# Kernel tuning notes

Measured on AMD Instinct MI355X. Metric: run time of the kernel, lower is better.

Reference implementation:

```python
import jax, jax.numpy as jnp
import numpy as np
from jax import lax

# 8-neighbor zero-pad offsets as (left, right, top, bottom), matching nn.ZeroPad2d args
PADS = [(0, 2, 0, 2), (1, 1, 0, 2), (2, 0, 0, 2), (0, 2, 1, 1),
        (2, 0, 1, 1), (0, 2, 2, 0), (1, 1, 2, 0), (2, 0, 2, 0)]
BN_EPS = 1e-5


def conv2d(x, w, pad):
    return lax.conv_general_dilated(x, w, (1, 1), [(pad, pad), (pad, pad)],
                                    dimension_numbers=('NCHW', 'OIHW', 'NCHW'))


def batchnorm(x, gamma, beta, mean, var):
    inv = gamma * lax.rsqrt(var + BN_EPS)
    return x * inv[None, :, None, None] + (beta - mean * inv)[None, :, None, None]


def resize_bilinear(x, oh, ow):
    # F.interpolate(mode='bilinear', align_corners=False)
    n, c, h, w = x.shape
    ys = jnp.clip((jnp.arange(oh, dtype=x.dtype) + 0.5) * (h / oh) - 0.5, 0.0, None)
    xs = jnp.clip((jnp.arange(ow, dtype=x.dtype) + 0.5) * (w / ow) - 0.5, 0.0, None)
    y0 = jnp.floor(ys); x0 = jnp.floor(xs)
    wy = (ys - y0)[:, None]; wx = (xs - x0)[None, :]
    y0i = jnp.clip(y0.astype(jnp.int32), 0, h - 1)
    y1i = jnp.clip(y0i + 1, 0, h - 1)
    x0i = jnp.clip(x0.astype(jnp.int32), 0, w - 1)
    x1i = jnp.clip(x0i + 1, 0, w - 1)
    r0 = x[:, :, y0i, :]; r1 = x[:, :, y1i, :]
    top = r0[:, :, :, x0i] * (1 - wx) + r0[:, :, :, x1i] * wx
    bot = r1[:, :, :, x0i] * (1 - wx) + r1[:, :, :, x1i] * wx
    return top * (1 - wy) + bot * wy


def lrwarp_error(left, disp, right):
    # Warp right image toward left using horizontal disparity (bilinear,
    # zero padding outside), then per-channel absolute photometric error.
    n, c, h, w = right.shape
    xs = jnp.arange(w, dtype=disp.dtype)[None, None, None, :] - disp  # [n,1,h,w]
    x0 = jnp.floor(xs)
    frac = xs - x0
    x0i = x0.astype(jnp.int32)
    x1i = x0i + 1
    v0 = ((x0i >= 0) & (x0i < w)).astype(right.dtype)
    v1 = ((x1i >= 0) & (x1i < w)).astype(right.dtype)
    x0c = jnp.broadcast_to(jnp.clip(x0i, 0, w - 1), (n, c, h, w))
    x1c = jnp.broadcast_to(jnp.clip(x1i, 0, w - 1), (n, c, h, w))
    g0 = jnp.take_along_axis(right, x0c, axis=3) * v0
    g1 = jnp.take_along_axis(right, x1c, axis=3) * v1
    warped = g0 * (1 - frac) + g1 * frac
    return jnp.abs(left - warped)


def setup_inputs() -> dict:
    key = jax.random.key(0)
    ks = jax.random.split(key, 16)
    N, H, W = 8, 256, 256
    inp = {
        'normal_estimation': jax.random.normal(ks[0], (N, 3, H, W), jnp.float32),
        'left_image': jax.random.uniform(ks[1], (N, 3, 512, 512), jnp.float32),
        'right_image': jax.random.uniform(ks[2], (N, 3, 512, 512), jnp.float32),
        'coarse_disparity': jax.random.uniform(ks[3], (N, 1, H, W), jnp.float32),
        'w1': jax.random.normal(ks[4], (32, 12, 3, 3), jnp.float32) * 0.1,
        'g1': jnp.ones((32,), jnp.float32), 'b1': jnp.zeros((32,), jnp.float32),
        'm1': jax.random.normal(ks[5], (32,), jnp.float32) * 0.01,
        'v1': jax.random.uniform(ks[6], (32,), jnp.float32, 0.5, 1.5),
        'w2': jax.random.normal(ks[7], (64, 32, 3, 3), jnp.float32) * 0.1,
        'g2': jnp.ones((64,), jnp.float32), 'b2': jnp.zeros((64,), jnp.float32),
        'm2': jax.random.normal(ks[8], (64,), jnp.float32) * 0.01,
        'v2': jax.random.uniform(ks[9], (64,), jnp.float32, 0.5, 1.5),
        'w3': jax.random.normal(ks[10], (8, 64, 1, 1), jnp.float32) * 0.1,
    }
    return inp


def _forward(normal_estimation, left_image, right_image, coarse_disparity,
             w1, g1, b1, m1, v1, w2, g2, b2, m2, v2, w3):
    H, W = coarse_disparity.shape[-2], coarse_disparity.shape[-1]
    cur_l = resize_bilinear(left_image, H, W)
    cur_r = resize_bilinear(right_image, H, W)
    disp_err = lrwarp_error(cur_l, coarse_disparity, cur_r)
    feats = jnp.concatenate([normal_estimation, cur_l, cur_r, disp_err], axis=1)
    x = jax.nn.relu(batchnorm(conv2d(feats, w1, 1), g1, b1, m1, v1))
    x = jax.nn.relu(batchnorm(conv2d(x, w2, 1), g2, b2, m2, v2))
    aff = jax.nn.relu(conv2d(x, w3, 0))  # [N,8,H,W]
    gate_p = jnp.stack([jnp.pad(aff[:, k], ((0, 0), (t, b), (l, r)))
                        for k, (l, r, t, b) in enumerate(PADS)], axis=1)
    d = coarse_disparity[:, 0]
    disp_p = jnp.stack([jnp.pad(d, ((0, 0), (t, b), (l, r)))
                        for (l, r, t, b) in PADS], axis=1)
    gate = jax.nn.softmax(gate_p, axis=1)
    prop = jnp.sum(gate * disp_p, axis=1, keepdims=True)[:, :, 1:-1, 1:-1]
    return prop * 0.3 + coarse_disparity * 0.7


def reference(normal_estimation, left_image, right_image, coarse_disparity,
              w1, g1, b1, m1, v1, w2, g2, b2, m2, v2, w3):
    return _forward(normal_estimation, left_image, right_image, coarse_disparity,
                    w1, g1, b1, m1, v1, w2, g2, b2, m2, v2, w3)
```

## Files before the change

### kernel.cpp

```cpp
#include <hip/hip_runtime.h>
#include <math.h>

#define NB 8
#define HH 256
#define WW 256
#define HW (HH*WW)

#define OFF_FEATS 0UL
#define OFF_X1B   16777216UL
#define OFF_AFFB  50331648UL
#define OFF_W1FB  58720256UL
#define OFF_B1FB  58732544UL
#define OFF_W2FB  58732672UL
#define OFF_B2FB  58769536UL
#define OFF_W3FB  58769792UL

typedef short  short8 __attribute__((ext_vector_type(8)));
typedef ushort u16x8  __attribute__((ext_vector_type(8)));
typedef ushort u16x4  __attribute__((ext_vector_type(4)));
typedef float  f32x4  __attribute__((ext_vector_type(4)));

__device__ __forceinline__ ushort f2bf(float x) {
  uint u = __float_as_uint(x);
  return (ushort)((u + 0x7FFFu + ((u >> 16) & 1u)) >> 16);
}
__device__ __forceinline__ float bf2f(ushort h) {
  uint u = ((uint)h) << 16;
  return __uint_as_float(u);
}

__global__ __launch_bounds__(256) void build_feats(
    const float* __restrict__ normal, const float* __restrict__ left,
    const float* __restrict__ right, const float* __restrict__ disp,
    const float* __restrict__ w1, const float* __restrict__ g1,
    const float* __restrict__ b1, const float* __restrict__ m1,
    const float* __restrict__ v1,
    const float* __restrict__ w2, const float* __restrict__ g2,
    const float* __restrict__ b2, const float* __restrict__ m2,
    const float* __restrict__ v2, const float* __restrict__ w3,
    char* __restrict__ wsb) {
  if (blockIdx.x >= 1024) {
    int idx = (blockIdx.x - 1024) * 256 + threadIdx.x;
    ushort* w1f = (ushort*)(wsb + OFF_W1FB);
    float* b1f  = (float*)(wsb + OFF_B1FB);
    ushort* w2f = (ushort*)(wsb + OFF_W2FB);
    float* b2f  = (float*)(wsb + OFF_B2FB);
    ushort* w3f = (ushort*)(wsb + OFF_W3FB);
    if (idx < 6144) {
      int jj = idx & 7;
      int lane = (idx >> 3) & 63;
      int mt = (idx >> 9) & 1;
      int s = idx >> 10;
      int ky = s >> 1, t = s & 1;
      int q = lane >> 4, lx = lane & 15;
      int k = q * 8 + jj;
      int dcol = k >> 4, ch = k & 15;
      int kx = t * 2 + dcol;
      int out = mt * 16 + lx;
      float inv = g1[out] / sqrtf(v1[out] + 1e-5f);
      float val = (ch < 12 && kx < 3) ? w1[((out * 12 + ch) * 3 + ky) * 3 + kx] * inv : 0.f;
      w1f[idx] = f2bf(val);
    }
    int j = idx - 6144;
    if (j >= 0 && j < 18432) {
      int kk   = j >> 11;
      int nt   = (j >> 9) & 3;
      int lane = (j >> 3) & 63;
      int jj   = j & 7;
      int q  = lane >> 4, lx = lane & 15;
      int cin = q * 8 + jj;
      int out = nt * 16 + lx;
      float inv = g2[out] / sqrtf(v2[out] + 1e-5f);
      w2f[j] = f2bf(w2[(out * 32 + cin) * 9 + kk] * inv);
      if (kk == 0 && q == 0 && jj == 0) b2f[out] = b2[out] - m2[out] * inv;
    }
    int k2 = idx - 24576;
    if (k2 >= 0 && k2 < 32) {
      float inv = g1[k2] / sqrtf(v1[k2] + 1e-5f);
      b1f[k2] = b1[k2] - m1[k2] * inv;
    }
    int k3 = idx - 24608;
    if (k3 >= 0 && k3 < 1024) {
      int jj = k3 & 7;
      int lane = (k3 >> 3) & 63;
      int slice = k3 >> 9;
      int q = lane >> 4, lx = lane & 15;
      int ch = slice * 32 + q * 8 + jj;
      w3f[k3] = (lx < 8) ? f2bf(w3[lx * 64 + ch]) : (ushort)0;
    }
    return;
  }
  int gid = blockIdx.x * 256 + threadIdx.x;
  int n = gid >> 15;
  int r = gid & 32767;
  int i = r >> 7;
  int jt = r & 127;
  int j0 = jt << 1;
  int i2 = i << 1;
  ushort* feats = (ushort*)(wsb + OFF_FEATS);
  ushort tmp[32];
#pragma unroll
  for (int c = 0; c < 3; ++c) {
    float2 nm = *(const float2*)(normal + (size_t)(n * 3 + c) * HW + i * 256 + j0);
    tmp[c] = f2bf(nm.x);
    tmp[16 + c] = f2bf(nm.y);
  }
  float cl[2][3];
#pragma unroll
  for (int c = 0; c < 3; ++c) {
    const float* Lp = left + ((size_t)(n * 3 + c) * 512 + i2) * 512 + (j0 << 1);
    float4 a0 = *(const float4*)Lp;
    float4 a1 = *(const float4*)(Lp + 512);
    cl[0][c] = 0.25f * (a0.x + a0.y + a1.x + a1.y);
    cl[1][c] = 0.25f * (a0.z + a0.w + a1.z + a1.w);
    tmp[3 + c] = f2bf(cl[0][c]);
    tmp[19 + c] = f2bf(cl[1][c]);
    const float* Rp = right + ((size_t)(n * 3 + c) * 512 + i2) * 512 + (j0 << 1);
    float4 b0 = *(const float4*)Rp;
    float4 b1v = *(const float4*)(Rp + 512);
    tmp[6 + c] = f2bf(0.25f * (b0.x + b0.y + b1v.x + b1v.y));
    tmp[22 + c] = f2bf(0.25f * (b0.z + b0.w + b1v.z + b1v.w));
  }
  float2 dp2 = *(const float2*)(disp + (size_t)n * HW + i * 256 + j0);
#pragma unroll
  for (int p = 0; p < 2; ++p) {
    int j = j0 + p;
    float d = p ? dp2.y : dp2.x;
    float xs = (float)j - d;
    float x0f = floorf(xs);
    float fr = xs - x0f;
    int ix0 = (int)x0f;
    int ix1 = ix0 + 1;
    float vm0 = (ix0 >= 0 && ix0 < WW) ? 1.f : 0.f;
    float vm1 = (ix1 >= 0 && ix1 < WW) ? 1.f : 0.f;
    int x0c = min(max(ix0, 0), WW - 1);
    int x1c = min(max(ix1, 0), WW - 1);
    bool adj = (x1c == x0c + 1);
    int xs2 = min(x0c + 1, WW - 1);
#pragma unroll
    for (int c = 0; c < 3; ++c) {
      const float* Rb = right + ((size_t)(n * 3 + c) * 512 + i2) * 512;
      float2 f0 = *(const float2*)(Rb + (x0c << 1));
      float2 f1 = *(const float2*)(Rb + (x0c << 1) + 512);
      float2 f2v = *(const float2*)(Rb + (xs2 << 1));
      float2 f3 = *(const float2*)(Rb + (xs2 << 1) + 512);
      float avg0 = 0.25f * (f0.x + f0.y + f1.x + f1.y);
      float avg1 = 0.25f * (f2v.x + f2v.y + f3.x + f3.y);
      float gg0 = avg0 * vm0;
      float gg1 = (adj ? avg1 : avg0) * vm1;
      float warped = gg0 * (1.f - fr) + gg1 * fr;
      tmp[p * 16 + 9 + c] = f2bf(fabsf(cl[p][c] - warped));
    }
  }
#pragma unroll
  for (int c = 12; c < 16; ++c) { tmp[c] = 0; tmp[16 + c] = 0; }
  size_t ob = ((size_t)(n * HW + i * 256 + j0)) * 16;
#pragma unroll
  for (int vv = 0; vv < 4; ++vv)
    *(u16x8*)&feats[ob + vv * 8] = *(u16x8*)&tmp[vv * 8];
}

__global__ __launch_bounds__(256) void conv1_kernel(char* __restrict__ wsb) {
  __shared__ ushort tile[688 * 8];
  const ushort* __restrict__ feats = (const ushort*)(wsb + OFF_FEATS);
  const short8* __restrict__ w1fv = (const short8*)(wsb + OFF_W1FB);
  const float* __restrict__ b1f = (const float*)(wsb + OFF_B1FB);
  ushort* x1 = (ushort*)(wsb + OFF_X1B);
  int blk = blockIdx.x;
  int n = blk >> 8;
  int t = blk & 255;
  int ty0 = (t >> 4) << 4;
  int tx0 = (t & 15) << 4;
  int tid = threadIdx.x;
  int lane = tid & 63;
  int wid = tid >> 6;
  int q = lane >> 4;
  int lx = lane & 15;
  short8 aw[2][6];
#pragma unroll
  for (int s = 0; s < 6; ++s)
#pragma unroll
    for (int mt = 0; mt < 2; ++mt) aw[mt][s] = w1fv[(s * 2 + mt) * 64 + lane];
  for (int e = tid; e < 684; e += 256) {
    int row = e / 38;
    int rem = e - row * 38;
    int col = rem >> 1;
    int cc = rem & 1;
    int gy = ty0 + row - 1, gx = tx0 + col - 1;
    u16x8 v = (u16x8)0;
    if (gy >= 0 && gy < HH && gx >= 0 && gx < WW)
      v = *(const u16x8*)&feats[(((size_t)(n * 256 + gy)) * 256 + gx) * 16 + cc * 8];
    int slot = e ^ ((e >> 3) & 7);
    *(u16x8*)&tile[slot * 8] = v;
  }
  __syncthreads();
  short8 bfrag[6][2];
#pragma unroll
  for (int dr = 0; dr < 6; ++dr)
#pragma unroll
    for (int tt = 0; tt < 2; ++tt) {
      int prow = wid * 4 + dr;
      int G = (prow * 19 + lx + tt * 2 + (q >> 1)) * 2 + (q & 1);
      int slot = G ^ ((G >> 3) & 7);
      bfrag[dr][tt] = *(const short8*)&tile[slot * 8];
    }
  f32x4 acc[4][2];
#pragma unroll
  for (int rowt = 0; rowt < 4; ++rowt)
#pragma unroll
    for (int mt = 0; mt < 2; ++mt) acc[rowt][mt] = (f32x4)0.f;
#pragma unroll
  for (int s = 0; s < 6; ++s) {
    int ky = s >> 1;
    int tt = s & 1;
#pragma unroll
    for (int rowt = 0; rowt < 4; ++rowt) {
      short8 b = bfrag[rowt + ky][tt];
      acc[rowt][0] = __builtin_amdgcn_mfma_f32_16x16x32_bf16(aw[0][s], b, acc[rowt][0], 0, 0, 0);
      acc[rowt][1] = __builtin_amdgcn_mfma_f32_16x16x32_bf16(aw[1][s], b, acc[rowt][1], 0, 0, 0);
    }
  }
#pragma unroll
  for (int rowt = 0; rowt < 4; ++rowt) {
    int gy = ty0 + wid * 4 + rowt;
    int gx = tx0 + lx;
    size_t pb = (((size_t)(n * 256 + gy)) * 256 + gx) * 32;
#pragma unroll
    for (int mt = 0; mt < 2; ++mt) {
      u16x4 pack;
#pragma unroll
      for (int r = 0; r < 4; ++r) {
        int ch = mt * 16 + q * 4 + r;
        pack[r] = f2bf(fmaxf(acc[rowt][mt][r] + b1f[ch], 0.f));
      }
      *(u16x4*)&x1[pb + mt * 16 + q * 4] = pack;
    }
  }
}

__global__ __launch_bounds__(256) void conv2_kernel(char* __restrict__ wsb) {
  __shared__ ushort smem[256 * 68];
  const ushort* __restrict__ x1 = (const ushort*)(wsb + OFF_X1B);
  const short8* __restrict__ w2fv = (const short8*)(wsb + OFF_W2FB);
  const float* __restrict__ b2f = (const float*)(wsb + OFF_B2FB);
  const short8* __restrict__ w3fv = (const short8*)(wsb + OFF_W3FB);
  ushort* aff = (ushort*)(wsb + OFF_AFFB);

  int blk = blockIdx.x;
  int n = blk >> 8;
  int t = blk & 255;
  int ty0 = (t >> 4) << 4;
  int tx0 = (t & 15) << 4;
  int tid = threadIdx.x;
  int lane = tid & 63;
  int wid = tid >> 6;
  int q = lane >> 4;
  int lx = lane & 15;

  short8 bw3[2];
  bw3[0] = w3fv[lane];
  bw3[1] = w3fv[64 + lane];

  for (int e = tid; e < 1296; e += 256) {
    int p = e >> 2;
    int c = e & 3;
    int y = p / 18;
    int x = p - y * 18;
    int gy = ty0 + y - 1, gx = tx0 + x - 1;
    u16x8 val = (u16x8)0;
    if (gy >= 0 && gy < HH && gx >= 0 && gx < WW)
      val = *(const u16x8*)&x1[(((size_t)(n * 256 + gy)) * 256 + gx) * 32 + c * 8];
    *(u16x8*)&smem[p * 36 + c * 8] = val;
  }
  __syncthreads();

  f32x4 acc[4][4];
#pragma unroll
  for (int mt = 0; mt < 4; ++mt)
#pragma unroll
    for (int nt = 0; nt < 4; ++nt) acc[mt][nt] = (f32x4)0.f;

#pragma unroll
  for (int kk = 0; kk < 9; ++kk) {
    int ky = kk / 3, kx = kk - ky * 3;
    short8 a[4], b[4];
#pragma unroll
    for (int mt = 0; mt < 4; ++mt) {
      int row = wid * 4 + mt;
      a[mt] = *(const short8*)&smem[((row + ky) * 18 + lx + kx) * 36 + q * 8];
    }
#pragma unroll
    for (int nt = 0; nt < 4; ++nt) b[nt] = w2fv[(kk * 4 + nt) * 64 + lane];
#pragma unroll
    for (int mt = 0; mt < 4; ++mt)
#pragma unroll
      for (int nt = 0; nt < 4; ++nt)
        acc[mt][nt] = __builtin_amdgcn_mfma_f32_16x16x32_bf16(a[mt], b[nt], acc[mt][nt], 0, 0, 0);
  }

  __syncthreads();
#pragma unroll
  for (int nt = 0; nt < 4; ++nt) {
    float bias = b2f[nt * 16 + lx];
#pragma unroll
    for (int mt = 0; mt < 4; ++mt) {
      int row = wid * 4 + mt;
#pragma unroll
      for (int r = 0; r < 4; ++r) {
        int p = row * 16 + q * 4 + r;
        float v = fmaxf(acc[mt][nt][r] + bias, 0.f);
        smem[p * 68 + nt * 16 + lx] = f2bf(v);
      }
    }
  }
  __syncthreads();

  f32x4 acc3[4];
#pragma unroll
  for (int mt = 0; mt < 4; ++mt) acc3[mt] = (f32x4)0.f;
#pragma unroll
  for (int mt = 0; mt < 4; ++mt) {
    int p = wid * 64 + mt * 16 + lx;
#pragma unroll
    for (int s = 0; s < 2; ++s) {
      short8 a3 = *(const short8*)&smem[p * 68 + s * 32 + q * 8];
      acc3[mt] = __builtin_amdgcn_mfma_f32_16x16x32_bf16(a3, bw3[s], acc3[mt], 0, 0, 0);
    }
  }
  if (lx < 8) {
#pragma unroll
    for (int mt = 0; mt < 4; ++mt) {
      int py = ty0 + wid * 4 + mt;
      int px = tx0 + q * 4;
      u16x4 pk;
#pragma unroll
      for (int r = 0; r < 4; ++r) pk[r] = f2bf(fmaxf(acc3[mt][r], 0.f));
      *(u16x4*)&aff[((size_t)(n * 8 + lx)) * HW + (size_t)py * WW + px] = pk;
    }
  }
}

__global__ __launch_bounds__(256) void final_kernel(const float* __restrict__ disp,
                                                    const char* __restrict__ wsb,
                                                    float* __restrict__ out) {
  int gid = blockIdx.x * 256 + threadIdx.x;
  int n = gid >> 14;
  int r = gid & 16383;
  int i = r >> 6;
  int j0 = (r & 63) << 2;
  const ushort* aff = (const ushort*)(wsb + OFF_AFFB);
  float d6[3][6];
#pragma unroll
  for (int rr = 0; rr < 3; ++rr) {
    int y = min(max(i + rr - 1, 0), HH - 1);
    const float* dp = disp + (size_t)n * HW + y * WW;
    float4 c4 = *(const float4*)(dp + j0);
    d6[rr][1] = c4.x; d6[rr][2] = c4.y; d6[rr][3] = c4.z; d6[rr][4] = c4.w;
    d6[rr][0] = dp[max(j0 - 1, 0)];
    d6[rr][5] = dp[min(j0 + 4, WW - 1)];
  }
  const int dy[8] = {1, 1, 1, 0, 0, -1, -1, -1};
  const int dx[8] = {1, 0, -1, 1, -1, 1, 0, -1};
  float g[8][4], dvv[8][4];
#pragma unroll
  for (int k = 0; k < 8; ++k) {
    int y = i + dy[k];
    bool vy = (y >= 0 && y < HH);
    int yc = min(max(y, 0), HH - 1);
    const ushort* ap = aff + ((size_t)(n * 8 + k)) * HW + (size_t)yc * WW;
    float w6[6];
    u16x4 c4 = *(const u16x4*)(ap + j0);
    w6[1] = bf2f(c4[0]); w6[2] = bf2f(c4[1]); w6[3] = bf2f(c4[2]); w6[4] = bf2f(c4[3]);
    w6[0] = bf2f(ap[max(j0 - 1, 0)]);
    w6[5] = bf2f(ap[min(j0 + 4, WW - 1)]);
    int rr = dy[k] + 1;
#pragma unroll
    for (int p = 0; p < 4; ++p) {
      int xp = j0 + p + dx[k];
      bool ok = vy && (xp >= 0) && (xp < WW);
      g[k][p] = ok ? w6[p + 1 + dx[k]] : 0.f;
      dvv[k][p] = ok ? d6[rr][p + 1 + dx[k]] : 0.f;
    }
  }
  float4 res;
#pragma unroll
  for (int p = 0; p < 4; ++p) {
    float m = g[0][p];
#pragma unroll
    for (int k = 1; k < 8; ++k) m = fmaxf(m, g[k][p]);
    float se = 0.f, sed = 0.f;
#pragma unroll
    for (int k = 0; k < 8; ++k) {
      float e = __expf(g[k][p] - m);
      se += e;
      sed += e * dvv[k][p];
    }
    float dc = d6[1][p + 1];
    (&res.x)[p] = 0.3f * (sed / se) + 0.7f * dc;
  }
  *(float4*)(out + (size_t)n * HW + i * WW + j0) = res;
}

extern "C" void kernel_launch(void* const* d_in, const int* in_sizes, int n_in,
                              void* d_out, int out_size, void* d_ws, size_t ws_size,
                              hipStream_t stream) {
  const float* normal = (const float*)d_in[0];
  const float* left   = (const float*)d_in[1];
  const float* right  = (const float*)d_in[2];
  const float* disp   = (const float*)d_in[3];
  const float* w1 = (const float*)d_in[4];
  const float* g1 = (const float*)d_in[5];
  const float* b1 = (const float*)d_in[6];
  const float* m1 = (const float*)d_in[7];
  const float* v1 = (const float*)d_in[8];
  const float* w2 = (const float*)d_in[9];
  const float* g2 = (const float*)d_in[10];
  const float* b2 = (const float*)d_in[11];
  const float* m2 = (const float*)d_in[12];
  const float* v2 = (const float*)d_in[13];
  const float* w3 = (const float*)d_in[14];
  char* wsb  = (char*)d_ws;
  float* out = (float*)d_out;

  hipLaunchKernelGGL(build_feats, dim3(1125), dim3(256), 0, stream,
                     normal, left, right, disp,
                     w1, g1, b1, m1, v1, w2, g2, b2, m2, v2, w3, wsb);
  hipLaunchKernelGGL(conv1_kernel, dim3(2048), dim3(256), 0, stream, wsb);
  hipLaunchKernelGGL(conv2_kernel, dim3(2048), dim3(256), 0, stream, wsb);
  hipLaunchKernelGGL(final_kernel, dim3(512), dim3(256), 0, stream, disp, wsb, out);
}
```

Before: 166.5 us.

## Fuse feature build, conv1 and conv2 into one tiled trunk kernel

Merges feature construction, conv1 and conv2/conv3 into a single per-tile kernel. Each block computes its features over a 20x20 halo region, runs conv1 over an 18x18 region into LDS, then applies conv2 and conv3 from shared memory. Weight preparation moves to its own small kernel. This removes the global round trips for the 16-channel feats and 32-channel x1 intermediates, plus one launch. The cost is recomputing halo features and conv1 outputs at tile borders, more LDS per block, and uncoalesced scalar gathers of the input images.

New measurement: 169.0 us. About the same (+1.5%).

```diff
diff --git a/kernel.cpp b/kernel.cpp
--- a/kernel.cpp
+++ b/kernel.cpp
@@ -6,14 +6,12 @@
 #define WW 256
 #define HW (HH*WW)
 
-#define OFF_FEATS 0UL
-#define OFF_X1B   16777216UL
-#define OFF_AFFB  50331648UL
-#define OFF_W1FB  58720256UL
-#define OFF_B1FB  58732544UL
-#define OFF_W2FB  58732672UL
-#define OFF_B2FB  58769536UL
-#define OFF_W3FB  58769792UL
+#define OFF_AFFB  0UL
+#define OFF_W1FB  8388608UL
+#define OFF_B1FB  8400896UL
+#define OFF_W2FB  8401024UL
+#define OFF_B2FB  8437888UL
+#define OFF_W3FB  8438144UL
 
 typedef short  short8 __attribute__((ext_vector_type(8)));
 typedef ushort u16x8  __attribute__((ext_vector_type(8)));
@@ -29,9 +27,7 @@
   return __uint_as_float(u);
 }
 
-__global__ __launch_bounds__(256) void build_feats(
-    const float* __restrict__ normal, const float* __restrict__ left,
-    const float* __restrict__ right, const float* __restrict__ disp,
+__global__ __launch_bounds__(256) void prep_weights(
     const float* __restrict__ w1, const float* __restrict__ g1,
     const float* __restrict__ b1, const float* __restrict__ m1,
     const float* __restrict__ v1,
@@ -39,133 +35,69 @@
     const float* __restrict__ b2, const float* __restrict__ m2,
     const float* __restrict__ v2, const float* __restrict__ w3,
     char* __restrict__ wsb) {
-  if (blockIdx.x >= 1024) {
-    int idx = (blockIdx.x - 1024) * 256 + threadIdx.x;
-    ushort* w1f = (ushort*)(wsb + OFF_W1FB);
-    float* b1f  = (float*)(wsb + OFF_B1FB);
-    ushort* w2f = (ushort*)(wsb + OFF_W2FB);
-    float* b2f  = (float*)(wsb + OFF_B2FB);
-    ushort* w3f = (ushort*)(wsb + OFF_W3FB);
-    if (idx < 6144) {
-      int jj = idx & 7;
-      int lane = (idx >> 3) & 63;
-      int mt = (idx >> 9) & 1;
-      int s = idx >> 10;
-      int ky = s >> 1, t = s & 1;
-      int q = lane >> 4, lx = lane & 15;
-      int k = q * 8 + jj;
-      int dcol = k >> 4, ch = k & 15;
-      int kx = t * 2 + dcol;
-      int out = mt * 16 + lx;
-      float inv = g1[out] / sqrtf(v1[out] + 1e-5f);
-      float val = (ch < 12 && kx < 3) ? w1[((out * 12 + ch) * 3 + ky) * 3 + kx] * inv : 0.f;
-      w1f[idx] = f2bf(val);
-    }
-    int j = idx - 6144;
-    if (j >= 0 && j < 18432) {
-      int kk   = j >> 11;
-      int nt   = (j >> 9) & 3;
-      int lane = (j >> 3) & 63;
-      int jj   = j & 7;
-      int q  = lane >> 4, lx = lane & 15;
-      int cin = q * 8 + jj;
-      int out = nt * 16 + lx;
-      float inv = g2[out] / sqrtf(v2[out] + 1e-5f);
-      w2f[j] = f2bf(w2[(out * 32 + cin) * 9 + kk] * inv);
-      if (kk == 0 && q == 0 && jj == 0) b2f[out] = b2[out] - m2[out] * inv;
-    }
-    int k2 = idx - 24576;
-    if (k2 >= 0 && k2 < 32) {
-      float inv = g1[k2] / sqrtf(v1[k2] + 1e-5f);
-      b1f[k2] = b1[k2] - m1[k2] * inv;
-    }
-    int k3 = idx - 24608;
-    if (k3 >= 0 && k3 < 1024) {
-      int jj = k3 & 7;
-      int lane = (k3 >> 3) & 63;
-      int slice = k3 >> 9;
-      int q = lane >> 4, lx = lane & 15;
-      int ch = slice * 32 + q * 8 + jj;
-      w3f[k3] = (lx < 8) ? f2bf(w3[lx * 64 + ch]) : (ushort)0;
-    }
-    return;
-  }
-  int gid = blockIdx.x * 256 + threadIdx.x;
-  int n = gid >> 15;
-  int r = gid & 32767;
-  int i = r >> 7;
-  int jt = r & 127;
-  int j0 = jt << 1;
-  int i2 = i << 1;
-  ushort* feats = (ushort*)(wsb + OFF_FEATS);
-  ushort tmp[32];
-#pragma unroll
-  for (int c = 0; c < 3; ++c) {
-    float2 nm = *(const float2*)(normal + (size_t)(n * 3 + c) * HW + i * 256 + j0);
-    tmp[c] = f2bf(nm.x);
-    tmp[16 + c] = f2bf(nm.y);
-  }
-  float cl[2][3];
-#pragma unroll
-  for (int c = 0; c < 3; ++c) {
-    const float* Lp = left + ((size_t)(n * 3 + c) * 512 + i2) * 512 + (j0 << 1);
-    float4 a0 = *(const float4*)Lp;
-    float4 a1 = *(const float4*)(Lp + 512);
-    cl[0][c] = 0.25f * (a0.x + a0.y + a1.x + a1.y);
-    cl[1][c] = 0.25f * (a0.z + a0.w + a1.z + a1.w);
-    tmp[3 + c] = f2bf(cl[0][c]);
-    tmp[19 + c] = f2bf(cl[1][c]);
-    const float* Rp = right + ((size_t)(n * 3 + c) * 512 + i2) * 512 + (j0 << 1);
-    float4 b0 = *(const float4*)Rp;
-    float4 b1v = *(const float4*)(Rp + 512);
-    tmp[6 + c] = f2bf(0.25f * (b0.x + b0.y + b1v.x + b1v.y));
-    tmp[22 + c] = f2bf(0.25f * (b0.z + b0.w + b1v.z + b1v.w));
-  }
-  float2 dp2 = *(const float2*)(disp + (size_t)n * HW + i * 256 + j0);
-#pragma unroll
-  for (int p = 0; p < 2; ++p) {
-    int j = j0 + p;
-    float d = p ? dp2.y : dp2.x;
-    float xs = (float)j - d;
-    float x0f = floorf(xs);
-    float fr = xs - x0f;
-    int ix0 = (int)x0f;
-    int ix1 = ix0 + 1;
-    float vm0 = (ix0 >= 0 && ix0 < WW) ? 1.f : 0.f;
-    float vm1 = (ix1 >= 0 && ix1 < WW) ? 1.f : 0.f;
-    int x0c = min(max(ix0, 0), WW - 1);
-    int x1c = min(max(ix1, 0), WW - 1);
-    bool adj = (x1c == x0c + 1);
-    int xs2 = min(x0c + 1, WW - 1);
-#pragma unroll
-    for (int c = 0; c < 3; ++c) {
-      const float* Rb = right + ((size_t)(n * 3 + c) * 512 + i2) * 512;
-      float2 f0 = *(const float2*)(Rb + (x0c << 1));
-      float2 f1 = *(const float2*)(Rb + (x0c << 1) + 512);
-      float2 f2v = *(const float2*)(Rb + (xs2 << 1));
-      float2 f3 = *(const float2*)(Rb + (xs2 << 1) + 512);
-      float avg0 = 0.25f * (f0.x + f0.y + f1.x + f1.y);
-      float avg1 = 0.25f * (f2v.x + f2v.y + f3.x + f3.y);
-      float gg0 = avg0 * vm0;
-      float gg1 = (adj ? avg1 : avg0) * vm1;
-      float warped = gg0 * (1.f - fr) + gg1 * fr;
-      tmp[p * 16 + 9 + c] = f2bf(fabsf(cl[p][c] - warped));
-    }
-  }
-#pragma unroll
-  for (int c = 12; c < 16; ++c) { tmp[c] = 0; tmp[16 + c] = 0; }
-  size_t ob = ((size_t)(n * HW + i * 256 + j0)) * 16;
-#pragma unroll
-  for (int vv = 0; vv < 4; ++vv)
-    *(u16x8*)&feats[ob + vv * 8] = *(u16x8*)&tmp[vv * 8];
-}
-
-__global__ __launch_bounds__(256) void conv1_kernel(char* __restrict__ wsb) {
-  __shared__ ushort tile[688 * 8];
-  const ushort* __restrict__ feats = (const ushort*)(wsb + OFF_FEATS);
+  int idx = blockIdx.x * 256 + threadIdx.x;
+  ushort* w1f = (ushort*)(wsb + OFF_W1FB);
+  float* b1f  = (float*)(wsb + OFF_B1FB);
+  ushort* w2f = (ushort*)(wsb + OFF_W2FB);
+  float* b2f  = (float*)(wsb + OFF_B2FB);
+  ushort* w3f = (ushort*)(wsb + OFF_W3FB);
+  if (idx < 6144) {
+    int jj = idx & 7;
+    int lane = (idx >> 3) & 63;
+    int nt = (idx >> 9) & 1;
+    int s = idx >> 10;
+    int ky = s >> 1, t = s & 1;
+    int q = lane >> 4, lx = lane & 15;
+    int k = q * 8 + jj;
+    int dcol = k >> 4, ch = k & 15;
+    int kx = t * 2 + dcol;
+    int out = nt * 16 + lx;
+    float inv = g1[out] / sqrtf(v1[out] + 1e-5f);
+    float val = (ch < 12 && kx < 3) ? w1[((out * 12 + ch) * 3 + ky) * 3 + kx] * inv : 0.f;
+    w1f[idx] = f2bf(val);
+  }
+  int j = idx - 6144;
+  if (j >= 0 && j < 18432) {
+    int kk   = j >> 11;
+    int nt   = (j >> 9) & 3;
+    int lane = (j >> 3) & 63;
+    int jj   = j & 7;
+    int q  = lane >> 4, lx = lane & 15;
+    int cin = q * 8 + jj;
+    int out = nt * 16 + lx;
+    float inv = g2[out] / sqrtf(v2[out] + 1e-5f);
+    w2f[j] = f2bf(w2[(out * 32 + cin) * 9 + kk] * inv);
+    if (kk == 0 && q == 0 && jj == 0) b2f[out] = b2[out] - m2[out] * inv;
+  }
+  int k2 = idx - 24576;
+  if (k2 >= 0 && k2 < 32) {
+    float inv = g1[k2] / sqrtf(v1[k2] + 1e-5f);
+    b1f[k2] = b1[k2] - m1[k2] * inv;
+  }
+  int k3 = idx - 24608;
+  if (k3 >= 0 && k3 < 1024) {
+    int jj = k3 & 7;
+    int lane = (k3 >> 3) & 63;
+    int slice = k3 >> 9;
+    int q = lane >> 4, lx = lane & 15;
+    int ch = slice * 32 + q * 8 + jj;
+    w3f[k3] = (lx < 8) ? f2bf(w3[lx * 64 + ch]) : (ushort)0;
+  }
+}
+
+__global__ __launch_bounds__(256) void trunk_kernel(
+    const float* __restrict__ normal, const float* __restrict__ left,
+    const float* __restrict__ right, const float* __restrict__ disp,
+    char* __restrict__ wsb) {
+  __shared__ ushort buf[18304];
+  ushort* x1t = buf + 6464;
   const short8* __restrict__ w1fv = (const short8*)(wsb + OFF_W1FB);
   const float* __restrict__ b1f = (const float*)(wsb + OFF_B1FB);
-  ushort* x1 = (ushort*)(wsb + OFF_X1B);
+  const short8* __restrict__ w2fv = (const short8*)(wsb + OFF_W2FB);
+  const float* __restrict__ b2f = (const float*)(wsb + OFF_B2FB);
+  const short8* __restrict__ w3fv = (const short8*)(wsb + OFF_W3FB);
+  ushort* aff = (ushort*)(wsb + OFF_AFFB);
+
   int blk = blockIdx.x;
   int n = blk >> 8;
   int t = blk & 255;
@@ -176,145 +108,152 @@
   int wid = tid >> 6;
   int q = lane >> 4;
   int lx = lane & 15;
-  short8 aw[2][6];
-#pragma unroll
-  for (int s = 0; s < 6; ++s)
-#pragma unroll
-    for (int mt = 0; mt < 2; ++mt) aw[mt][s] = w1fv[(s * 2 + mt) * 64 + lane];
-  for (int e = tid; e < 684; e += 256) {
-    int row = e / 38;
-    int rem = e - row * 38;
-    int col = rem >> 1;
-    int cc = rem & 1;
-    int gy = ty0 + row - 1, gx = tx0 + col - 1;
-    u16x8 v = (u16x8)0;
-    if (gy >= 0 && gy < HH && gx >= 0 && gx < WW)
-      v = *(const u16x8*)&feats[(((size_t)(n * 256 + gy)) * 256 + gx) * 16 + cc * 8];
-    int slot = e ^ ((e >> 3) & 7);
-    *(u16x8*)&tile[slot * 8] = v;
+
+  if (tid < 8) *(u16x8*)&buf[(800 + tid) * 8] = (u16x8)0;
+  for (int e = tid; e < 400; e += 256) {
+    int row = e / 20, col = e - row * 20;
+    int gy = ty0 + row - 2, gx = tx0 + col - 2;
+    ushort tmp[16];
+#pragma unroll
+    for (int c = 12; c < 16; ++c) tmp[c] = 0;
+    if (gy >= 0 && gy < HH && gx >= 0 && gx < WW) {
+#pragma unroll
+      for (int c = 0; c < 3; ++c)
+        tmp[c] = f2bf(normal[(size_t)(n * 3 + c) * HW + gy * WW + gx]);
+      int i2 = gy << 1, j2 = gx << 1;
+      float cl[3];
+#pragma unroll
+      for (int c = 0; c < 3; ++c) {
+        const float* Lp = left + ((size_t)(n * 3 + c) * 512 + i2) * 512 + j2;
+        float2 a0 = *(const float2*)Lp;
+        float2 a1 = *(const float2*)(Lp + 512);
+        cl[c] = 0.25f * (a0.x + a0.y + a1.x + a1.y);
+        tmp[3 + c] = f2bf(cl[c]);
+        const float* Rp = right + ((size_t)(n * 3 + c) * 512 + i2) * 512 + j2;
+        float2 b0 = *(const float2*)Rp;
+        float2 b1v = *(const float2*)(Rp + 512);
+        tmp[6 + c] = f2bf(0.25f * (b0.x + b0.y + b1v.x + b1v.y));
+      }
+      float d = disp[(size_t)n * HW + gy * WW + gx];
+      float xs = (float)gx - d;
+      float x0f = floorf(xs);
+      float fr = xs - x0f;
+      int ix0 = (int)x0f;
+      int ix1 = ix0 + 1;
+      float vm0 = (ix0 >= 0 && ix0 < WW) ? 1.f : 0.f;
+      float vm1 = (ix1 >= 0 && ix1 < WW) ? 1.f : 0.f;
+      int x0c = min(max(ix0, 0), WW - 1);
+      int x1c = min(max(ix1, 0), WW - 1);
+      bool adj = (x1c == x0c + 1);
+      int xs2 = min(x0c + 1, WW - 1);
+#pragma unroll
+      for (int c = 0; c < 3; ++c) {
+        const float* Rb = right + ((size_t)(n * 3 + c) * 512 + i2) * 512;
+        float2 f0 = *(const float2*)(Rb + (x0c << 1));
+        float2 f1 = *(const float2*)(Rb + (x0c << 1) + 512);
+        float2 f2v = *(const float2*)(Rb + (xs2 << 1));
+        float2 f3 = *(const float2*)(Rb + (xs2 << 1) + 512);
+        float avg0 = 0.25f * (f0.x + f0.y + f1.x + f1.y);
+        float avg1 = 0.25f * (f2v.x + f2v.y + f3.x + f3.y);
+        float gg0 = avg0 * vm0;
+        float gg1 = (adj ? avg1 : avg0) * vm1;
+        float warped = gg0 * (1.f - fr) + gg1 * fr;
+        tmp[9 + c] = f2bf(fabsf(cl[c] - warped));
+      }
+    } else {
+#pragma unroll
+      for (int c = 0; c < 12; ++c) tmp[c] = 0;
+    }
+    int G0 = e * 2, G1 = G0 + 1;
+    int s0 = G0 ^ ((G0 >> 3) & 7);
+    int s1 = G1 ^ ((G1 >> 3) & 7);
+    *(u16x8*)&buf[s0 * 8] = *(u16x8*)&tmp[0];
+    *(u16x8*)&buf[s1 * 8] = *(u16x8*)&tmp[8];
   }
   __syncthreads();
-  short8 bfrag[6][2];
-#pragma unroll
-  for (int dr = 0; dr < 6; ++dr)
-#pragma unroll
-    for (int tt = 0; tt < 2; ++tt) {
-      int prow = wid * 4 + dr;
-      int G = (prow * 19 + lx + tt * 2 + (q >> 1)) * 2 + (q & 1);
-      int slot = G ^ ((G >> 3) & 7);
-      bfrag[dr][tt] = *(const short8*)&tile[slot * 8];
-    }
-  f32x4 acc[4][2];
-#pragma unroll
-  for (int rowt = 0; rowt < 4; ++rowt)
-#pragma unroll
-    for (int mt = 0; mt < 2; ++mt) acc[rowt][mt] = (f32x4)0.f;
-#pragma unroll
-  for (int s = 0; s < 6; ++s) {
-    int ky = s >> 1;
-    int tt = s & 1;
-#pragma unroll
-    for (int rowt = 0; rowt < 4; ++rowt) {
-      short8 b = bfrag[rowt + ky][tt];
-      acc[rowt][0] = __builtin_amdgcn_mfma_f32_16x16x32_bf16(aw[0][s], b, acc[rowt][0], 0, 0, 0);
-      acc[rowt][1] = __builtin_amdgcn_mfma_f32_16x16x32_bf16(aw[1][s], b, acc[rowt][1], 0, 0, 0);
-    }
-  }
-#pragma unroll
-  for (int rowt = 0; rowt < 4; ++rowt) {
-    int gy = ty0 + wid * 4 + rowt;
-    int gx = tx0 + lx;
-    size_t pb = (((size_t)(n * 256 + gy)) * 256 + gx) * 32;
-#pragma unroll
-    for (int mt = 0; mt < 2; ++mt) {
-      u16x4 pack;
+
+  {
+    short8 bw1[6][2];
+#pragma unroll
+    for (int s = 0; s < 6; ++s)
+#pragma unroll
+      for (int nt = 0; nt < 2; ++nt) bw1[s][nt] = w1fv[(s * 2 + nt) * 64 + lane];
+    float bias1[2] = {b1f[lx], b1f[16 + lx]};
+    for (int m = wid; m < 21; m += 4) {
+      int pidx = min(m * 16 + lx, 323);
+      int oyr = pidx / 18, oxr = pidx - oyr * 18;
+      f32x4 a1[2];
+      a1[0] = (f32x4)0.f; a1[1] = (f32x4)0.f;
+#pragma unroll
+      for (int s = 0; s < 6; ++s) {
+        int ky = s >> 1, tt = s & 1;
+        int G = ((oyr + ky) * 20 + oxr + tt * 2 + (q >> 1)) * 2 + (q & 1);
+        int slot = G ^ ((G >> 3) & 7);
+        short8 a = *(const short8*)&buf[slot * 8];
+        a1[0] = __builtin_amdgcn_mfma_f32_16x16x32_bf16(a, bw1[s][0], a1[0], 0, 0, 0);
+        a1[1] = __builtin_amdgcn_mfma_f32_16x16x32_bf16(a, bw1[s][1], a1[1], 0, 0, 0);
+      }
 #pragma unroll
       for (int r = 0; r < 4; ++r) {
-        int ch = mt * 16 + q * 4 + r;
-        pack[r] = f2bf(fmaxf(acc[rowt][mt][r] + b1f[ch], 0.f));
-      }
-      *(u16x4*)&x1[pb + mt * 16 + q * 4] = pack;
-    }
-  }
-}
-
-__global__ __launch_bounds__(256) void conv2_kernel(char* __restrict__ wsb) {
-  __shared__ ushort smem[256 * 68];
-  const ushort* __restrict__ x1 = (const ushort*)(wsb + OFF_X1B);
-  const short8* __restrict__ w2fv = (const short8*)(wsb + OFF_W2FB);
-  const float* __restrict__ b2f = (const float*)(wsb + OFF_B2FB);
-  const short8* __restrict__ w3fv = (const short8*)(wsb + OFF_W3FB);
-  ushort* aff = (ushort*)(wsb + OFF_AFFB);
-
-  int blk = blockIdx.x;
-  int n = blk >> 8;
-  int t = blk & 255;
-  int ty0 = (t >> 4) << 4;
-  int tx0 = (t & 15) << 4;
-  int tid = threadIdx.x;
-  int lane = tid & 63;
-  int wid = tid >> 6;
-  int q = lane >> 4;
-  int lx = lane & 15;
+        int p2 = m * 16 + q * 4 + r;
+        if (p2 < 324) {
+          int ry = p2 / 18, rx = p2 - ry * 18;
+          int gy = ty0 + ry - 1, gx = tx0 + rx - 1;
+          bool okp = (gy >= 0 && gy < HH && gx >= 0 && gx < WW);
+#pragma unroll
+          for (int nt = 0; nt < 2; ++nt) {
+            float v = okp ? fmaxf(a1[nt][r] + bias1[nt], 0.f) : 0.f;
+            x1t[(ry * 18 + rx) * 36 + nt * 16 + lx] = f2bf(v);
+          }
+        }
+      }
+    }
+  }
+  __syncthreads();
+
+  f32x4 acc[4][4];
+#pragma unroll
+  for (int mt = 0; mt < 4; ++mt)
+#pragma unroll
+    for (int nt = 0; nt < 4; ++nt) acc[mt][nt] = (f32x4)0.f;
+#pragma unroll
+  for (int kk = 0; kk < 9; ++kk) {
+    int ky = kk / 3, kx = kk - ky * 3;
+    short8 a[4], b[4];
+#pragma unroll
+    for (int mt = 0; mt < 4; ++mt) {
+      int row = wid * 4 + mt;
+      a[mt] = *(const short8*)&x1t[((row + ky) * 18 + lx + kx) * 36 + q * 8];
+    }
+#pragma unroll
+    for (int nt = 0; nt < 4; ++nt) b[nt] = w2fv[(kk * 4 + nt) * 64 + lane];
+#pragma unroll
+    for (int mt = 0; mt < 4; ++mt)
+#pragma unroll
+      for (int nt = 0; nt < 4; ++nt)
+        acc[mt][nt] = __builtin_amdgcn_mfma_f32_16x16x32_bf16(a[mt], b[nt], acc[mt][nt], 0, 0, 0);
+  }
+  __syncthreads();
+
+#pragma unroll
+  for (int nt = 0; nt < 4; ++nt) {
+    float bias = b2f[nt * 16 + lx];
+#pragma unroll
+    for (int mt = 0; mt < 4; ++mt) {
+      int row = wid * 4 + mt;
+#pragma unroll
+      for (int r = 0; r < 4; ++r) {
+        int p = row * 16 + q * 4 + r;
+        float v = fmaxf(acc[mt][nt][r] + bias, 0.f);
+        buf[p * 68 + nt * 16 + lx] = f2bf(v);
+      }
+    }
+  }
+  __syncthreads();
 
   short8 bw3[2];
   bw3[0] = w3fv[lane];
   bw3[1] = w3fv[64 + lane];
-
-  for (int e = tid; e < 1296; e += 256) {
-    int p = e >> 2;
-    int c = e & 3;
-    int y = p / 18;
-    int x = p - y * 18;
-    int gy = ty0 + y - 1, gx = tx0 + x - 1;
-    u16x8 val = (u16x8)0;
-    if (gy >= 0 && gy < HH && gx >= 0 && gx < WW)
-      val = *(const u16x8*)&x1[(((size_t)(n * 256 + gy)) * 256 + gx) * 32 + c * 8];
-    *(u16x8*)&smem[p * 36 + c * 8] = val;
-  }
-  __syncthreads();
-
-  f32x4 acc[4][4];
-#pragma unroll
-  for (int mt = 0; mt < 4; ++mt)
-#pragma unroll
-    for (int nt = 0; nt < 4; ++nt) acc[mt][nt] = (f32x4)0.f;
-
-#pragma unroll
-  for (int kk = 0; kk < 9; ++kk) {
-    int ky = kk / 3, kx = kk - ky * 3;
-    short8 a[4], b[4];
-#pragma unroll
-    for (int mt = 0; mt < 4; ++mt) {
-      int row = wid * 4 + mt;
-      a[mt] = *(const short8*)&smem[((row + ky) * 18 + lx + kx) * 36 + q * 8];
-    }
-#pragma unroll
-    for (int nt = 0; nt < 4; ++nt) b[nt] = w2fv[(kk * 4 + nt) * 64 + lane];
-#pragma unroll
-    for (int mt = 0; mt < 4; ++mt)
-#pragma unroll
-      for (int nt = 0; nt < 4; ++nt)
-        acc[mt][nt] = __builtin_amdgcn_mfma_f32_16x16x32_bf16(a[mt], b[nt], acc[mt][nt], 0, 0, 0);
-  }
-
-  __syncthreads();
-#pragma unroll
-  for (int nt = 0; nt < 4; ++nt) {
-    float bias = b2f[nt * 16 + lx];
-#pragma unroll
-    for (int mt = 0; mt < 4; ++mt) {
-      int row = wid * 4 + mt;
-#pragma unroll
-      for (int r = 0; r < 4; ++r) {
-        int p = row * 16 + q * 4 + r;
-        float v = fmaxf(acc[mt][nt][r] + bias, 0.f);
-        smem[p * 68 + nt * 16 + lx] = f2bf(v);
-      }
-    }
-  }
-  __syncthreads();
-
   f32x4 acc3[4];
 #pragma unroll
   for (int mt = 0; mt < 4; ++mt) acc3[mt] = (f32x4)0.f;
@@ -323,7 +262,7 @@
     int p = wid * 64 + mt * 16 + lx;
 #pragma unroll
     for (int s = 0; s < 2; ++s) {
-      short8 a3 = *(const short8*)&smem[p * 68 + s * 32 + q * 8];
+      short8 a3 = *(const short8*)&buf[p * 68 + s * 32 + q * 8];
       acc3[mt] = __builtin_amdgcn_mfma_f32_16x16x32_bf16(a3, bw3[s], acc3[mt], 0, 0, 0);
     }
   }
@@ -422,10 +361,9 @@
   char* wsb  = (char*)d_ws;
   float* out = (float*)d_out;
 
-  hipLaunchKernelGGL(build_feats, dim3(1125), dim3(256), 0, stream,
-                     normal, left, right, disp,
+  hipLaunchKernelGGL(prep_weights, dim3(101), dim3(256), 0, stream,
                      w1, g1, b1, m1, v1, w2, g2, b2, m2, v2, w3, wsb);
-  hipLaunchKernelGGL(conv1_kernel, dim3(2048), dim3(256), 0, stream, wsb);
-  hipLaunchKernelGGL(conv2_kernel, dim3(2048), dim3(256), 0, stream, wsb);
+  hipLaunchKernelGGL(trunk_kernel, dim3(2048), dim3(256), 0, stream,
+                     normal, left, right, disp, wsb);
   hipLaunchKernelGGL(final_kernel, dim3(512), dim3(256), 0, stream, disp, wsb, out);
 }
```
